# Kernel tuning notes

Hardware: AMD Instinct MI355X
Metric: run time of the kernel (lower is better)

## Reference

```python
import jax, jax.numpy as jnp
import numpy as np

N, E, D, H, C = 50000, 800000, 128, 1, 128  # nodes, edges, in_dim, heads, hidden
NEG_SLOPE = 0.2


def setup_inputs() -> dict:
    key = jax.random.key(0)
    ks = jax.random.split(key, 12)
    x = jax.random.normal(ks[0], (N, D), dtype=jnp.float32)
    edge_index = jax.random.randint(ks[1], (2, E), 0, N, dtype=jnp.int64)
    s = 1.0 / np.sqrt(D)
    inp = {"x": x, "edge_index": edge_index}
    for i, base in [(1, 2), (2, 7)]:
        inp[f"W{i}"] = jax.random.normal(ks[base], (D, H * C), dtype=jnp.float32) * s
        inp[f"att_src{i}"] = jax.random.normal(ks[base + 1], (H, C), dtype=jnp.float32) * s
        inp[f"att_dst{i}"] = jax.random.normal(ks[base + 2], (H, C), dtype=jnp.float32) * s
        inp[f"b{i}"] = jnp.zeros((C,), dtype=jnp.float32)
    return inp


def _gat_layer(x, src, dst, W, att_src, att_dst, b):
    n = x.shape[0]
    xl = (x @ W).reshape(n, H, C)                      # [N,H,C]
    a_s = jnp.sum(xl * att_src, axis=-1)               # [N,H]
    a_d = jnp.sum(xl * att_dst, axis=-1)               # [N,H]
    e = jax.nn.leaky_relu(a_s[src] + a_d[dst], NEG_SLOPE)  # [E',H]
    # segment softmax over incoming edges of each dst node
    m = jax.ops.segment_max(e, dst, num_segments=n)
    e = jnp.exp(e - m[dst])
    z = jax.ops.segment_sum(e, dst, num_segments=n)
    alpha = e / (z[dst] + 1e-16)                       # [E',H]
    msg = xl[src] * alpha[:, :, None]                  # [E',H,C]
    out = jax.ops.segment_sum(msg, dst, num_segments=n)  # [N,H,C]
    return out.mean(axis=1) + b                        # concat=False -> head mean


def reference(x, edge_index, W1, att_src1, att_dst1, b1, W2, att_src2, att_dst2, b2):
    # PyG GATConv default add_self_loops=True
    loops = jnp.arange(N, dtype=edge_index.dtype)
    src = jnp.concatenate([edge_index[0], loops])
    dst = jnp.concatenate([edge_index[1], loops])
    h = _gat_layer(x, src, dst, W1, att_src1, att_dst1, b1)
    h = jax.nn.relu(h)
    h = _gat_layer(h, src, dst, W2, att_src2, att_dst2, b2)
    return jax.nn.relu(h)
```

## Files before the change

### kernel.cpp

```cpp
#include <hip/hip_runtime.h>
#include <hip/hip_bf16.h>
#include <math.h>

#define NEG_SLOPE 0.2f

using bf16x8 = __attribute__((ext_vector_type(8))) short;
using f32x4 = __attribute__((ext_vector_type(4))) float;

__device__ __forceinline__ float lrelu(float v) {
    return v > 0.0f ? v : NEG_SLOPE * v;
}

__device__ __forceinline__ float wred_sum(float v) {
    #pragma unroll
    for (int d = 32; d; d >>= 1) v += __shfl_xor(v, d);
    return v;
}

__device__ __forceinline__ unsigned short f2bf(float f) {
    unsigned u = __float_as_uint(f);
    return (unsigned short)((u + 0x7FFFu + ((u >> 16) & 1u)) >> 16);
}

__device__ __forceinline__ void bf8_fma(float* acc, uint4 u, float w) {
    acc[0] += w * __uint_as_float(u.x << 16);
    acc[1] += w * __uint_as_float(u.x & 0xFFFF0000u);
    acc[2] += w * __uint_as_float(u.y << 16);
    acc[3] += w * __uint_as_float(u.y & 0xFFFF0000u);
    acc[4] += w * __uint_as_float(u.z << 16);
    acc[5] += w * __uint_as_float(u.z & 0xFFFF0000u);
    acc[6] += w * __uint_as_float(u.w << 16);
    acc[7] += w * __uint_as_float(u.w & 0xFFFF0000u);
}

__global__ void k_init(const float* __restrict__ W1, const float* __restrict__ W2,
                       unsigned short* __restrict__ h1, unsigned short* __restrict__ l1,
                       unsigned short* __restrict__ h2, unsigned short* __restrict__ l2,
                       int* __restrict__ counts, int n4) {
    int b = blockIdx.x;
    if (b < 128) {
        int i = b * 256 + threadIdx.x;
        int sel = i >> 14;
        int j = i & 16383;
        int nn = j >> 7, kk = j & 127;
        const float* W = sel ? W2 : W1;
        float f = W[kk * 128 + nn];
        unsigned short h = f2bf(f);
        float hf = __uint_as_float((unsigned)h << 16);
        unsigned short lo = f2bf(f - hf);
        if (sel) { h2[j] = h; l2[j] = lo; }
        else     { h1[j] = h; l1[j] = lo; }
    } else {
        int i = (b - 128) * 256 + threadIdx.x;
        if (i < n4) ((int4*)counts)[i] = make_int4(0, 0, 0, 0);
    }
}

__global__ void k_hist_rank8(const int* __restrict__ dst, int E,
                             int* __restrict__ counts, int* __restrict__ rank) {
    int i = blockIdx.x * blockDim.x + threadIdx.x;
    int base = i << 3;
    if (base + 7 < E) {
        int4 d0 = ((const int4*)dst)[i * 2];
        int4 d1 = ((const int4*)dst)[i * 2 + 1];
        int4 r0, r1;
        r0.x = atomicAdd(&counts[d0.x], 1);
        r0.y = atomicAdd(&counts[d0.y], 1);
        r0.z = atomicAdd(&counts[d0.z], 1);
        r0.w = atomicAdd(&counts[d0.w], 1);
        r1.x = atomicAdd(&counts[d1.x], 1);
        r1.y = atomicAdd(&counts[d1.y], 1);
        r1.z = atomicAdd(&counts[d1.z], 1);
        r1.w = atomicAdd(&counts[d1.w], 1);
        ((int4*)rank)[i * 2] = r0;
        ((int4*)rank)[i * 2 + 1] = r1;
    } else {
        for (int j = base; j < E; ++j) rank[j] = atomicAdd(&counts[dst[j]], 1);
    }
}

__global__ void k_hist_rank_s(const int* __restrict__ dst, int E,
                              int* __restrict__ counts, int* __restrict__ rank) {
    int i = blockIdx.x * blockDim.x + threadIdx.x;
    if (i < E) rank[i] = atomicAdd(&counts[dst[i]], 1);
}

__global__ __launch_bounds__(1024) void k_scan(const int* __restrict__ counts,
                                               int* __restrict__ offsets, int n) {
    __shared__ int wsums[16];
    __shared__ int carry_sh;
    int tid = threadIdx.x;
    int lane = tid & 63;
    int wv = tid >> 6;
    if (tid == 0) carry_sh = 0;
    int n4 = (n + 3) >> 2;
    int4 c = (tid < n4) ? ((const int4*)counts)[tid] : make_int4(0, 0, 0, 0);
    __syncthreads();
    for (int base = 0; base < n4; base += 1024) {
        int i = base + tid;
        int inx = i + 1024;
        int4 cn = (inx < n4) ? ((const int4*)counts)[inx] : make_int4(0, 0, 0, 0);
        int p1 = c.x, p2 = p1 + c.y, p3 = p2 + c.z, tot = p3 + c.w;
        int x = tot;
        #pragma unroll
        for (int d = 1; d < 64; d <<= 1) {
            int y = __shfl_up(x, d);
            if (lane >= d) x += y;
        }
        if (lane == 63) wsums[wv] = x;
        __syncthreads();
        if (wv == 0) {
            int s = (lane < 16) ? wsums[lane] : 0;
            #pragma unroll
            for (int d = 1; d < 16; d <<= 1) {
                int y = __shfl_up(s, d);
                if (lane >= d) s += y;
            }
            if (lane < 16) wsums[lane] = s;
        }
        __syncthreads();
        int excl = carry_sh + (wv > 0 ? wsums[wv - 1] : 0) + (x - tot);
        if (i < n4)
            ((int4*)offsets)[i] = make_int4(excl, excl + p1, excl + p2, excl + p3);
        __syncthreads();
        if (tid == 0) carry_sh += wsums[15];
        c = cn;
        __syncthreads();
    }
    if (tid == 0) offsets[n] = carry_sh;
}

__global__ void k_scatter8(const int* __restrict__ src, const int* __restrict__ dst,
                           const int* __restrict__ rank, const int* __restrict__ offsets,
                           int E, int* __restrict__ csr_src) {
    int i = blockIdx.x * blockDim.x + threadIdx.x;
    int base = i << 3;
    if (base + 7 < E) {
        int4 s0 = ((const int4*)src)[i * 2];
        int4 s1 = ((const int4*)src)[i * 2 + 1];
        int4 d0 = ((const int4*)dst)[i * 2];
        int4 d1 = ((const int4*)dst)[i * 2 + 1];
        int4 r0 = ((const int4*)rank)[i * 2];
        int4 r1 = ((const int4*)rank)[i * 2 + 1];
        csr_src[offsets[d0.x] + r0.x] = s0.x;
        csr_src[offsets[d0.y] + r0.y] = s0.y;
        csr_src[offsets[d0.z] + r0.z] = s0.z;
        csr_src[offsets[d0.w] + r0.w] = s0.w;
        csr_src[offsets[d1.x] + r1.x] = s1.x;
        csr_src[offsets[d1.y] + r1.y] = s1.y;
        csr_src[offsets[d1.z] + r1.z] = s1.z;
        csr_src[offsets[d1.w] + r1.w] = s1.w;
    } else {
        for (int j = base; j < E; ++j) csr_src[offsets[dst[j]] + rank[j]] = src[j];
    }
}

__global__ void k_scatter_s(const int* __restrict__ src, const int* __restrict__ dst,
                            const int* __restrict__ rank, const int* __restrict__ offsets,
                            int E, int* __restrict__ csr_src) {
    int i = blockIdx.x * blockDim.x + threadIdx.x;
    if (i < E) csr_src[offsets[dst[i]] + rank[i]] = src[i];
}

__global__ __launch_bounds__(256) void k_gemm_attn(const float* __restrict__ X,
                                                   const unsigned short* __restrict__ Wth,
                                                   const unsigned short* __restrict__ Wtl,
                                                   const float* __restrict__ att_s,
                                                   const float* __restrict__ att_d,
                                                   unsigned short* __restrict__ XLb,
                                                   float* __restrict__ a_s,
                                                   float* __restrict__ a_d, int n) {
    __shared__ unsigned short WhT[8192];
    __shared__ unsigned short WlT[8192];
    __shared__ unsigned short XhT[8192];
    __shared__ unsigned short XlT[8192];
    __shared__ float pS[2][128];
    __shared__ float pD[2][128];

    const int tid = threadIdx.x;
    const int row0 = blockIdx.x * 128;
    const int wave = tid >> 6;
    const int l = tid & 63;
    const int lr = l & 15;
    const int lg = l >> 4;
    const int qm = (wave & 1) * 64;
    const int qn = (wave >> 1) * 64;
    const unsigned swz = (unsigned)(l & 7) << 4;

    f32x4 acc[4][4];
    #pragma unroll
    for (int a = 0; a < 4; ++a)
        #pragma unroll
        for (int b = 0; b < 4; ++b)
            acc[a][b] = (f32x4){0.f, 0.f, 0.f, 0.f};

    for (int kb = 0; kb < 128; kb += 64) {
        __syncthreads();
        #pragma unroll
        for (int it = 0; it < 4; ++it) {
            int idx = it * 256 + tid;
            int m = idx >> 3;
            int kc = idx & 7;
            int gr = row0 + m;
            float4 v0 = make_float4(0.f, 0.f, 0.f, 0.f), v1 = v0;
            if (gr < n) {
                const float4* Xp = (const float4*)X + (size_t)gr * 32 + (kb >> 2) + (kc << 1);
                v0 = Xp[0];
                v1 = Xp[1];
            }
            float fv[8] = {v0.x, v0.y, v0.z, v0.w, v1.x, v1.y, v1.z, v1.w};
            unsigned hp[4], lp[4];
            #pragma unroll
            for (int e = 0; e < 4; ++e) {
                unsigned short h0 = f2bf(fv[2 * e]);
                unsigned short h1 = f2bf(fv[2 * e + 1]);
                float r0 = fv[2 * e] - __uint_as_float((unsigned)h0 << 16);
                float r1 = fv[2 * e + 1] - __uint_as_float((unsigned)h1 << 16);
                hp[e] = (unsigned)h0 | ((unsigned)h1 << 16);
                lp[e] = (unsigned)f2bf(r0) | ((unsigned)f2bf(r1) << 16);
            }
            unsigned off = ((unsigned)m << 7) + ((unsigned)kc << 4);
            unsigned so = off ^ (((unsigned)m & 7) << 4);
            *(uint4*)((char*)XhT + so) = make_uint4(hp[0], hp[1], hp[2], hp[3]);
            *(uint4*)((char*)XlT + so) = make_uint4(lp[0], lp[1], lp[2], lp[3]);
            size_t wsrc = (size_t)m * 128 + kb + (kc << 3);
            *(uint4*)((char*)WhT + so) = *(const uint4*)(Wth + wsrc);
            *(uint4*)((char*)WlT + so) = *(const uint4*)(Wtl + wsrc);
        }
        __syncthreads();
        #pragma unroll
        for (int ks = 0; ks < 64; ks += 32) {
            bf16x8 ah[4], al[4];
            #pragma unroll
            for (int mt = 0; mt < 4; ++mt) {
                unsigned ao = (((unsigned)(qm + mt * 16 + lr)) << 7) +
                              ((unsigned)ks << 1) + ((unsigned)lg << 4);
                ao ^= swz;
                ah[mt] = *(const bf16x8*)((const char*)WhT + ao);
                al[mt] = *(const bf16x8*)((const char*)WlT + ao);
            }
            #pragma unroll
            for (int nt = 0; nt < 4; ++nt) {
                unsigned bo = (((unsigned)(qn + nt * 16 + lr)) << 7) +
                              ((unsigned)ks << 1) + ((unsigned)lg << 4);
                bo ^= swz;
                bf16x8 bh = *(const bf16x8*)((const char*)XhT + bo);
                bf16x8 bl = *(const bf16x8*)((const char*)XlT + bo);
                #pragma unroll
                for (int mt = 0; mt < 4; ++mt) {
                    acc[mt][nt] = __builtin_amdgcn_mfma_f32_16x16x32_bf16(ah[mt], bh, acc[mt][nt], 0, 0, 0);
                    acc[mt][nt] = __builtin_amdgcn_mfma_f32_16x16x32_bf16(al[mt], bh, acc[mt][nt], 0, 0, 0);
                    acc[mt][nt] = __builtin_amdgcn_mfma_f32_16x16x32_bf16(ah[mt], bl, acc[mt][nt], 0, 0, 0);
                }
            }
        }
    }

    float4 asv[4], adv[4];
    #pragma unroll
    for (int mt = 0; mt < 4; ++mt) {
        asv[mt] = *(const float4*)&att_s[qm + mt * 16 + (lg << 2)];
        adv[mt] = *(const float4*)&att_d[qm + mt * 16 + (lg << 2)];
    }
    #pragma unroll
    for (int nt = 0; nt < 4; ++nt) {
        float ps = 0.f, pd = 0.f;
        #pragma unroll
        for (int mt = 0; mt < 4; ++mt) {
            f32x4 a = acc[mt][nt];
            ps += a[0] * asv[mt].x + a[1] * asv[mt].y + a[2] * asv[mt].z + a[3] * asv[mt].w;
            pd += a[0] * adv[mt].x + a[1] * adv[mt].y + a[2] * adv[mt].z + a[3] * adv[mt].w;
        }
        ps += __shfl_xor(ps, 16); ps += __shfl_xor(ps, 32);
        pd += __shfl_xor(pd, 16); pd += __shfl_xor(pd, 32);
        if (l < 16) {
            pS[wave & 1][qn + nt * 16 + l] = ps;
            pD[wave & 1][qn + nt * 16 + l] = pd;
        }
    }
    #pragma unroll
    for (int nt = 0; nt < 4; ++nt) {
        int grow = row0 + qn + nt * 16 + lr;
        if (grow < n) {
            #pragma unroll
            for (int mt = 0; mt < 4; ++mt) {
                int col = qm + mt * 16 + (lg << 2);
                f32x4 a = acc[mt][nt];
                unsigned p0 = ((unsigned)f2bf(a[1]) << 16) | f2bf(a[0]);
                unsigned p1 = ((unsigned)f2bf(a[3]) << 16) | f2bf(a[2]);
                *(uint2*)(XLb + (size_t)grow * 128 + col) = make_uint2(p0, p1);
            }
        }
    }
    __syncthreads();
    if (tid < 128) {
        int gr = row0 + tid;
        if (gr < n) {
            a_s[gr] = pS[0][tid] + pS[1][tid];
            a_d[gr] = pD[0][tid] + pD[1][tid];
        }
    }
}

__global__ __launch_bounds__(256) void k_aggregate(const unsigned short* __restrict__ xlb,
                                                   const float* __restrict__ a_s,
                                                   const float* __restrict__ a_d,
                                                   const int* __restrict__ csr_src,
                                                   const int* __restrict__ offsets,
                                                   const float* __restrict__ bias,
                                                   float* __restrict__ out, int n) {
    int wid = (blockIdx.x * blockDim.x + threadIdx.x) >> 6;
    int lane = threadIdx.x & 63;
    if (wid >= n) return;
    int beg = offsets[wid];
    int deg = offsets[wid + 1] - beg;
    float a_dn = a_d[wid];
    float w_self = __expf(lrelu(a_s[wid] + a_dn));

    int s_l = 0;
    float w_l = 0.0f;
    if (lane < deg) {
        s_l = csr_src[beg + lane];
        w_l = __expf(lrelu(a_s[s_l] + a_dn));
    }
    float zl = w_l;
    for (int j = 64 + lane; j < deg; j += 64) {
        int s = csr_src[beg + j];
        zl += __expf(lrelu(a_s[s] + a_dn));
    }
    float z = wred_sum(zl) + w_self;
    float inv = 1.0f / (z + 1e-16f);

    int qw = lane >> 4, ql = lane & 15;
    const uint4* xb4 = (const uint4*)xlb;
    float acc[8] = {};
    if (qw == 0) {
        uint4 u = xb4[(size_t)wid * 16 + ql];
        bf8_fma(acc, u, w_self);
    }
    int jmax = deg < 64 ? deg : 64;
    int nt = (jmax + 7) >> 3;
    for (int t = 0; t < nt; ++t) {
        int ja = (t << 3) + qw;
        int jb = ja + 4;
        int jca = ja < jmax ? ja : 0;
        int jcb = jb < jmax ? jb : 0;
        float wa = __shfl(w_l, jca);
        int sa = __shfl(s_l, jca);
        float wb = __shfl(w_l, jcb);
        int sb = __shfl(s_l, jcb);
        if (ja >= jmax) wa = 0.0f;
        if (jb >= jmax) wb = 0.0f;
        uint4 ua = xb4[(size_t)sa * 16 + ql];
        uint4 ub = xb4[(size_t)sb * 16 + ql];
        bf8_fma(acc, ua, wa);
        bf8_fma(acc, ub, wb);
    }
    for (int j = 64 + qw; j < deg; j += 4) {
        int sj = csr_src[beg + j];
        float wj = __expf(lrelu(a_s[sj] + a_dn));
        uint4 u = xb4[(size_t)sj * 16 + ql];
        bf8_fma(acc, u, wj);
    }
    #pragma unroll
    for (int k = 0; k < 8; ++k) {
        acc[k] += __shfl_xor(acc[k], 16);
        acc[k] += __shfl_xor(acc[k], 32);
    }
    if (qw == 0) {
        float4 b0 = ((const float4*)bias)[ql * 2];
        float4 b1 = ((const float4*)bias)[ql * 2 + 1];
        float4 r0, r1;
        r0.x = fmaxf(acc[0] * inv + b0.x, 0.0f);
        r0.y = fmaxf(acc[1] * inv + b0.y, 0.0f);
        r0.z = fmaxf(acc[2] * inv + b0.z, 0.0f);
        r0.w = fmaxf(acc[3] * inv + b0.w, 0.0f);
        r1.x = fmaxf(acc[4] * inv + b1.x, 0.0f);
        r1.y = fmaxf(acc[5] * inv + b1.y, 0.0f);
        r1.z = fmaxf(acc[6] * inv + b1.z, 0.0f);
        r1.w = fmaxf(acc[7] * inv + b1.w, 0.0f);
        ((float4*)out)[(size_t)wid * 32 + ql * 2] = r0;
        ((float4*)out)[(size_t)wid * 32 + ql * 2 + 1] = r1;
    }
}

extern "C" void kernel_launch(void* const* d_in, const int* in_sizes, int n_in,
                              void* d_out, int out_size, void* d_ws, size_t ws_size,
                              hipStream_t stream) {
    const float* x = (const float*)d_in[0];
    const int* edges = (const int*)d_in[1];
    const float* W1 = (const float*)d_in[2];
    const float* att_s1 = (const float*)d_in[3];
    const float* att_d1 = (const float*)d_in[4];
    const float* b1 = (const float*)d_in[5];
    const float* W2 = (const float*)d_in[6];
    const float* att_s2 = (const float*)d_in[7];
    const float* att_d2 = (const float*)d_in[8];
    const float* b2 = (const float*)d_in[9];

    const int N = in_sizes[0] / 128;
    const int E = in_sizes[1] / 2;
    const int* e_src = edges;
    const int* e_dst = edges + E;

    char* w = (char*)d_ws;
    auto carve = [&](size_t bytes) {
        char* p = w;
        w += (bytes + 255) & ~(size_t)255;
        return p;
    };
    const int n4 = (N + 3) >> 2;
    int* counts = (int*)carve((size_t)n4 * 16);
    int* offsets = (int*)carve((size_t)(N + 8) * 4);
    int* rank = (int*)carve((size_t)E * 4);
    int* csr_src = (int*)carve((size_t)E * 4);
    float* a_s = (float*)carve((size_t)N * 4);
    float* a_d = (float*)carve((size_t)N * 4);
    unsigned short* xlb = (unsigned short*)carve((size_t)N * 128 * 2);
    float* h = (float*)carve((size_t)N * 128 * 4);
    unsigned short* wth1 = (unsigned short*)carve(16384 * 2);
    unsigned short* wtl1 = (unsigned short*)carve(16384 * 2);
    unsigned short* wth2 = (unsigned short*)carve(16384 * 2);
    unsigned short* wtl2 = (unsigned short*)carve(16384 * 2);

    float* out = (float*)d_out;

    int init_blocks = 128 + (n4 + 255) / 256;
    k_init<<<init_blocks, 256, 0, stream>>>(W1, W2, wth1, wtl1, wth2, wtl2, counts, n4);

    bool vec_ok = ((((uintptr_t)e_dst) & 15) == 0) && ((((uintptr_t)e_src) & 15) == 0);
    if (vec_ok) {
        int qb = ((E + 7) / 8 + 255) / 256;
        k_hist_rank8<<<qb, 256, 0, stream>>>(e_dst, E, counts, rank);
        k_scan<<<1, 1024, 0, stream>>>(counts, offsets, N);
        k_scatter8<<<qb, 256, 0, stream>>>(e_src, e_dst, rank, offsets, E, csr_src);
    } else {
        int sb = (E + 255) / 256;
        k_hist_rank_s<<<sb, 256, 0, stream>>>(e_dst, E, counts, rank);
        k_scan<<<1, 1024, 0, stream>>>(counts, offsets, N);
        k_scatter_s<<<sb, 256, 0, stream>>>(e_src, e_dst, rank, offsets, E, csr_src);
    }

    int gemm_blocks = (N + 127) / 128;
    int wave_blocks = (N * 64 + 255) / 256;

    k_gemm_attn<<<gemm_blocks, 256, 0, stream>>>(x, wth1, wtl1, att_s1, att_d1, xlb, a_s, a_d, N);
    k_aggregate<<<wave_blocks, 256, 0, stream>>>(xlb, a_s, a_d, csr_src, offsets, b1, h, N);

    k_gemm_attn<<<gemm_blocks, 256, 0, stream>>>(h, wth2, wtl2, att_s2, att_d2, xlb, a_s, a_d, N);
    k_aggregate<<<wave_blocks, 256, 0, stream>>>(xlb, a_s, a_d, csr_src, offsets, b2, out, N);
}
```

Before: 178.1 us.

## Co-schedule edge histogram with layer-1 GEMM in one interleaved kernel launch

Merges the edge-degree histogram/rank kernel and the first-layer projection GEMM into a single launch whose blocks alternate between the two roles. The atomic-bound histogram and the matrix-core GEMM are independent, so running them concurrently on the GPU is meant to overlap their latencies and remove one launch boundary. The combined kernel carries the GEMM's large shared-memory footprint for histogram blocks too, which can reduce how many histogram blocks fit per CU.

```diff
diff --git a/kernel.cpp b/kernel.cpp
--- a/kernel.cpp
+++ b/kernel.cpp
@@ -53,29 +53,6 @@
     } else {
         int i = (b - 128) * 256 + threadIdx.x;
         if (i < n4) ((int4*)counts)[i] = make_int4(0, 0, 0, 0);
-    }
-}
-
-__global__ void k_hist_rank8(const int* __restrict__ dst, int E,
-                             int* __restrict__ counts, int* __restrict__ rank) {
-    int i = blockIdx.x * blockDim.x + threadIdx.x;
-    int base = i << 3;
-    if (base + 7 < E) {
-        int4 d0 = ((const int4*)dst)[i * 2];
-        int4 d1 = ((const int4*)dst)[i * 2 + 1];
-        int4 r0, r1;
-        r0.x = atomicAdd(&counts[d0.x], 1);
-        r0.y = atomicAdd(&counts[d0.y], 1);
-        r0.z = atomicAdd(&counts[d0.z], 1);
-        r0.w = atomicAdd(&counts[d0.w], 1);
-        r1.x = atomicAdd(&counts[d1.x], 1);
-        r1.y = atomicAdd(&counts[d1.y], 1);
-        r1.z = atomicAdd(&counts[d1.z], 1);
-        r1.w = atomicAdd(&counts[d1.w], 1);
-        ((int4*)rank)[i * 2] = r0;
-        ((int4*)rank)[i * 2 + 1] = r1;
-    } else {
-        for (int j = base; j < E; ++j) rank[j] = atomicAdd(&counts[dst[j]], 1);
     }
 }
 
@@ -162,14 +139,14 @@
     if (i < E) csr_src[offsets[dst[i]] + rank[i]] = src[i];
 }
 
-__global__ __launch_bounds__(256) void k_gemm_attn(const float* __restrict__ X,
-                                                   const unsigned short* __restrict__ Wth,
-                                                   const unsigned short* __restrict__ Wtl,
-                                                   const float* __restrict__ att_s,
-                                                   const float* __restrict__ att_d,
-                                                   unsigned short* __restrict__ XLb,
-                                                   float* __restrict__ a_s,
-                                                   float* __restrict__ a_d, int n) {
+__device__ void gemm_attn_body(const float* __restrict__ X,
+                               const unsigned short* __restrict__ Wth,
+                               const unsigned short* __restrict__ Wtl,
+                               const float* __restrict__ att_s,
+                               const float* __restrict__ att_d,
+                               unsigned short* __restrict__ XLb,
+                               float* __restrict__ a_s,
+                               float* __restrict__ a_d, int n, int row0) {
     __shared__ unsigned short WhT[8192];
     __shared__ unsigned short WlT[8192];
     __shared__ unsigned short XhT[8192];
@@ -178,7 +155,6 @@
     __shared__ float pD[2][128];
 
     const int tid = threadIdx.x;
-    const int row0 = blockIdx.x * 128;
     const int wave = tid >> 6;
     const int l = tid & 63;
     const int lr = l & 15;
@@ -300,6 +276,59 @@
             a_d[gr] = pD[0][tid] + pD[1][tid];
         }
     }
+}
+
+__global__ __launch_bounds__(256) void k_hist_gemm(
+        const int* __restrict__ dst, int E,
+        int* __restrict__ counts, int* __restrict__ rank,
+        const float* __restrict__ X,
+        const unsigned short* __restrict__ Wth,
+        const unsigned short* __restrict__ Wtl,
+        const float* __restrict__ att_s, const float* __restrict__ att_d,
+        unsigned short* __restrict__ XLb,
+        float* __restrict__ a_s, float* __restrict__ a_d,
+        int n, int ng, int nh) {
+    int b = blockIdx.x;
+    int mn = ng < nh ? ng : nh;
+    int two = 2 * mn;
+    int role, rid;
+    if (b < two) { role = b & 1; rid = b >> 1; }
+    else { role = (ng > nh) ? 0 : 1; rid = mn + (b - two); }
+
+    if (role == 0) {
+        gemm_attn_body(X, Wth, Wtl, att_s, att_d, XLb, a_s, a_d, n, rid * 128);
+    } else {
+        int i = rid * 256 + (int)threadIdx.x;
+        int base = i << 3;
+        if (base + 7 < E) {
+            int4 d0 = ((const int4*)dst)[i * 2];
+            int4 d1 = ((const int4*)dst)[i * 2 + 1];
+            int4 r0, r1;
+            r0.x = atomicAdd(&counts[d0.x], 1);
+            r0.y = atomicAdd(&counts[d0.y], 1);
+            r0.z = atomicAdd(&counts[d0.z], 1);
+            r0.w = atomicAdd(&counts[d0.w], 1);
+            r1.x = atomicAdd(&counts[d1.x], 1);
+            r1.y = atomicAdd(&counts[d1.y], 1);
+            r1.z = atomicAdd(&counts[d1.z], 1);
+            r1.w = atomicAdd(&counts[d1.w], 1);
+            ((int4*)rank)[i * 2] = r0;
+            ((int4*)rank)[i * 2 + 1] = r1;
+        } else {
+            for (int j = base; j < E; ++j) rank[j] = atomicAdd(&counts[dst[j]], 1);
+        }
+    }
+}
+
+__global__ __launch_bounds__(256) void k_gemm_attn(const float* __restrict__ X,
+                                                   const unsigned short* __restrict__ Wth,
+                                                   const unsigned short* __restrict__ Wtl,
+                                                   const float* __restrict__ att_s,
+                                                   const float* __restrict__ att_d,
+                                                   unsigned short* __restrict__ XLb,
+                                                   float* __restrict__ a_s,
+                                                   float* __restrict__ a_d, int n) {
+    gemm_attn_body(X, Wth, Wtl, att_s, att_d, XLb, a_s, a_d, n, blockIdx.x * 128);
 }
 
 __global__ __launch_bounds__(256) void k_aggregate(const unsigned short* __restrict__ xlb,
@@ -428,23 +457,26 @@
     int init_blocks = 128 + (n4 + 255) / 256;
     k_init<<<init_blocks, 256, 0, stream>>>(W1, W2, wth1, wtl1, wth2, wtl2, counts, n4);
 
+    int gemm_blocks = (N + 127) / 128;
+    int wave_blocks = (N * 64 + 255) / 256;
+
     bool vec_ok = ((((uintptr_t)e_dst) & 15) == 0) && ((((uintptr_t)e_src) & 15) == 0);
     if (vec_ok) {
+        int nh = ((E + 7) / 8 + 255) / 256;
+        k_hist_gemm<<<nh + gemm_blocks, 256, 0, stream>>>(
+            e_dst, E, counts, rank,
+            x, wth1, wtl1, att_s1, att_d1, xlb, a_s, a_d, N, gemm_blocks, nh);
+        k_scan<<<1, 1024, 0, stream>>>(counts, offsets, N);
         int qb = ((E + 7) / 8 + 255) / 256;
-        k_hist_rank8<<<qb, 256, 0, stream>>>(e_dst, E, counts, rank);
-        k_scan<<<1, 1024, 0, stream>>>(counts, offsets, N);
         k_scatter8<<<qb, 256, 0, stream>>>(e_src, e_dst, rank, offsets, E, csr_src);
     } else {
         int sb = (E + 255) / 256;
         k_hist_rank_s<<<sb, 256, 0, stream>>>(e_dst, E, counts, rank);
+        k_gemm_attn<<<gemm_blocks, 256, 0, stream>>>(x, wth1, wtl1, att_s1, att_d1, xlb, a_s, a_d, N);
         k_scan<<<1, 1024, 0, stream>>>(counts, offsets, N);
         k_scatter_s<<<sb, 256, 0, stream>>>(e_src, e_dst, rank, offsets, E, csr_src);
     }
 
-    int gemm_blocks = (N + 127) / 128;
-    int wave_blocks = (N * 64 + 255) / 256;
-
-    k_gemm_attn<<<gemm_blocks, 256, 0, stream>>>(x, wth1, wtl1, att_s1, att_d1, xlb, a_s, a_d, N);
     k_aggregate<<<wave_blocks, 256, 0, stream>>>(xlb, a_s, a_d, csr_src, offsets, b1, h, N);
 
     k_gemm_attn<<<gemm_blocks, 256, 0, stream>>>(h, wth2, wtl2, att_s2, att_d2, xlb, a_s, a_d, N);
```

Result: slower. 182.8 us, median of 2 (+2.6%).
